# Kernel optimization log

Measured on AMD Instinct MI355X. Metric: run time of the kernel, lower is better.

## Reference

```python
import jax, jax.numpy as jnp
import numpy as np

B, T, S = 4, 2048, 2048
D, H, DFF = 1024, 16, 4096
HD = D // H
EPS = 1e-5


def layer_norm(x, gamma, beta):
    mean = x.mean(-1, keepdims=True)
    var = ((x - mean) ** 2).mean(-1, keepdims=True)
    return gamma * (x - mean) / jnp.sqrt(var + EPS) + beta


def attn(q, k, v):
    # q: [B,H,Tq,hd], k,v: [B,H,Tk,hd]
    scores = jnp.einsum('bhqd,bhkd->bhqk', q, k) / (HD ** 0.5)
    p = jax.nn.softmax(scores, axis=-1)
    return jnp.einsum('bhqk,bhkd->bhqd', p, v)


def split_heads(x, n_chunks):
    # x: [B,T,n_chunks*D] -> n_chunks tensors [B,H,T,hd] (matches torch reshape/chunk order)
    b, t, _ = x.shape
    x = x.reshape(b, t, H, n_chunks * HD).transpose(0, 2, 1, 3)
    return jnp.split(x, n_chunks, axis=-1)


def merge_heads(x):
    b, h, t, hd = x.shape
    return x.transpose(0, 2, 1, 3).reshape(b, t, h * hd)


def setup_inputs() -> dict:
    key = jax.random.key(0)
    ks = jax.random.split(key, 16)
    s = 0.02
    return {
        'x_enc': jax.random.normal(ks[0], (B, S, D), jnp.float32),
        'x_dec': jax.random.normal(ks[1], (B, T, D), jnp.float32),
        'qkv_w': jax.random.normal(ks[2], (D, 3 * D), jnp.float32) * s,
        'qkv_b': jnp.zeros((3 * D,), jnp.float32),
        'sa_o_w': jax.random.normal(ks[3], (D, D), jnp.float32) * s,
        'sa_o_b': jnp.zeros((D,), jnp.float32),
        'g1': jnp.ones((D,), jnp.float32),
        'be1': jnp.zeros((D,), jnp.float32),
        'q_w': jax.random.normal(ks[4], (D, D), jnp.float32) * s,
        'q_b': jnp.zeros((D,), jnp.float32),
        'kv_w': jax.random.normal(ks[5], (D, 2 * D), jnp.float32) * s,
        'kv_b': jnp.zeros((2 * D,), jnp.float32),
        'ca_o_w': jax.random.normal(ks[6], (D, D), jnp.float32) * s,
        'ca_o_b': jnp.zeros((D,), jnp.float32),
        'g2': jnp.ones((D,), jnp.float32),
        'be2': jnp.zeros((D,), jnp.float32),
        'ff_w1': jax.random.normal(ks[7], (D, DFF), jnp.float32) * s,
        'ff_b1': jnp.zeros((DFF,), jnp.float32),
        'ff_w2': jax.random.normal(ks[8], (DFF, D), jnp.float32) * s,
        'ff_b2': jnp.zeros((D,), jnp.float32),
        'g3': jnp.ones((D,), jnp.float32),
        'be3': jnp.zeros((D,), jnp.float32),
    }


def reference(x_enc, x_dec, qkv_w, qkv_b, sa_o_w, sa_o_b, g1, be1,
              q_w, q_b, kv_w, kv_b, ca_o_w, ca_o_b, g2, be2,
              ff_w1, ff_b1, ff_w2, ff_b2, g3, be3):
    # --- self attention on x_dec (dropout = identity at inference) ---
    qkv = x_dec @ qkv_w + qkv_b                      # [B,T,3D]
    q, k, v = split_heads(qkv, 3)
    sa = merge_heads(attn(q, k, v)) @ sa_o_w + sa_o_b
    res = layer_norm(sa + x_dec, g1, be1)
    # --- cross attention: q from decoder stream, kv from encoder ---
    kv = x_enc @ kv_w + kv_b                         # [B,S,2D]
    kc, vc = split_heads(kv, 2)
    qc, = split_heads(res @ q_w + q_b, 1)
    ca = merge_heads(attn(qc, kc, vc)) @ ca_o_w + ca_o_b
    res2 = layer_norm(ca + res, g2, be2)
    # --- feed forward ---
    ff = jax.nn.relu(res2 @ ff_w1 + ff_b1) @ ff_w2 + ff_b2
    return layer_norm(ff + res2, g3, be3)
```

## Files before the change

kernel.cpp:

```cpp
#include <hip/hip_runtime.h>

typedef unsigned short u16;
typedef unsigned int   u32;
typedef __bf16 bf16_t;
typedef bf16_t bf16x4 __attribute__((ext_vector_type(4)));
typedef bf16_t bf16x8 __attribute__((ext_vector_type(8)));
typedef float  f32x4  __attribute__((ext_vector_type(4)));

__device__ __forceinline__ u16 f2bf(float f) {
  u32 u = __builtin_bit_cast(u32, f);
  u32 r = u + 0x7fffu + ((u >> 16) & 1u);
  return (u16)(r >> 16);
}
__device__ __forceinline__ float bf2f(u16 h) {
  u32 u = ((u32)h) << 16;
  return __builtin_bit_cast(float, u);
}

__device__ __forceinline__ void gl_lds16(const u16* g, u16* l) {
  __builtin_amdgcn_global_load_lds(
      (const __attribute__((address_space(1))) u32*)g,
      (__attribute__((address_space(3))) u32*)l, 16, 0, 0);
}

__global__ __launch_bounds__(256) void k_cvt(const float* __restrict__ in,
                                             u16* __restrict__ out, long n4) {
  long i = (long)blockIdx.x * 256 + threadIdx.x;
  if (i >= n4) return;
  float4 v = reinterpret_cast<const float4*>(in)[i];
  ushort4 o;
  o.x = f2bf(v.x); o.y = f2bf(v.y); o.z = f2bf(v.z); o.w = f2bf(v.w);
  reinterpret_cast<ushort4*>(out)[i] = o;
}

__global__ __launch_bounds__(256) void k_transpose_cvt(const float* __restrict__ W,
                                                       u16* __restrict__ Wt,
                                                       int K, int N) {
  __shared__ u16 tile[32][33];
  int n0 = blockIdx.x * 32, k0 = blockIdx.y * 32;
  int tx = threadIdx.x & 31, ty = threadIdx.x >> 5;
#pragma unroll
  for (int i = 0; i < 4; ++i) {
    int k = ty + i * 8;
    tile[k][tx] = f2bf(W[(size_t)(k0 + k) * N + n0 + tx]);
  }
  __syncthreads();
#pragma unroll
  for (int i = 0; i < 4; ++i) {
    int n = ty + i * 8;
    Wt[(size_t)(n0 + n) * K + k0 + tx] = tile[tx][n];
  }
}

__global__ __launch_bounds__(256) void k_vtrans(const u16* __restrict__ in,
                                                u16* __restrict__ out,
                                                long long ibs, int ihs, int irs,
                                                int Tk) {
  __shared__ u16 t[64][72];
  const int tid = threadIdx.x;
  const int head = blockIdx.y;
  const int b = head >> 4, h = head & 15;
  const int kt = blockIdx.x * 64;
  const u16* ip = in + (size_t)b * ibs + (size_t)h * ihs;
  u16* op = out + (size_t)head * 64 * Tk;
#pragma unroll
  for (int i = 0; i < 2; ++i) {
    int c = i * 256 + tid;
    int key = c >> 3, d = (c & 7) * 8;
    *reinterpret_cast<uint4*>(&t[key][d]) =
        *reinterpret_cast<const uint4*>(ip + (size_t)(kt + key) * irs + d);
  }
  __syncthreads();
#pragma unroll
  for (int i = 0; i < 2; ++i) {
    int c = i * 256 + tid;
    int d = c >> 3, k8 = (c & 7) * 8;
    ushort4 lo, hi;
    lo.x = t[k8 + 0][d]; lo.y = t[k8 + 1][d]; lo.z = t[k8 + 2][d]; lo.w = t[k8 + 3][d];
    hi.x = t[k8 + 4][d]; hi.y = t[k8 + 5][d]; hi.z = t[k8 + 6][d]; hi.w = t[k8 + 7][d];
    uint4 o;
    o.x = ((u32)lo.y << 16) | lo.x; o.y = ((u32)lo.w << 16) | lo.z;
    o.z = ((u32)hi.y << 16) | hi.x; o.w = ((u32)hi.w << 16) | hi.z;
    *reinterpret_cast<uint4*>(op + (size_t)d * Tk + kt + k8) = o;
  }
}

template<int RELU>
__global__ __launch_bounds__(256) void k_gemm_bt(
    const u16* __restrict__ A, const u16* __restrict__ Bt,
    const float* __restrict__ bias, u16* __restrict__ C,
    int M, int N, int K)
{
  __shared__ __align__(16) u16 As[2][128 * 64];
  __shared__ __align__(16) u16 Bs[2][128 * 64];
  const int tid = threadIdx.x;
  const int lane = tid & 63, wid = tid >> 6;
  const int wr = wid >> 1, wc = wid & 1;
  const int l15 = lane & 15, g = lane >> 4;
  const int bm = blockIdx.x * 128, bn = blockIdx.y * 128;
  const int srow = lane >> 3, scol = (lane & 7) * 8;

  f32x4 acc[4][4] = {};

  auto stage = [&](int buf, int kt) {
#pragma unroll
    for (int i = 0; i < 4; ++i) {
      int ch = wid * 4 + i;
      gl_lds16(A  + (size_t)(bm + ch * 8 + srow) * K + kt + scol, &As[buf][ch * 512]);
      gl_lds16(Bt + (size_t)(bn + ch * 8 + srow) * K + kt + scol, &Bs[buf][ch * 512]);
    }
  };

  stage(0, 0);
  __syncthreads();
  int cur = 0;
  for (int kt = 0; kt < K; kt += 64) {
    if (kt + 64 < K) stage(cur ^ 1, kt + 64);
#pragma unroll
    for (int ks = 0; ks < 2; ++ks) {
      bf16x8 af[4], bfr[4];
#pragma unroll
      for (int m = 0; m < 4; ++m)
        af[m] = *reinterpret_cast<const bf16x8*>(&As[cur][(wr * 64 + m * 16 + l15) * 64 + ks * 32 + g * 8]);
#pragma unroll
      for (int n = 0; n < 4; ++n)
        bfr[n] = *reinterpret_cast<const bf16x8*>(&Bs[cur][(wc * 64 + n * 16 + l15) * 64 + ks * 32 + g * 8]);
      __builtin_amdgcn_s_setprio(1);
#pragma unroll
      for (int m = 0; m < 4; ++m)
#pragma unroll
        for (int n = 0; n < 4; ++n)
          acc[m][n] = __builtin_amdgcn_mfma_f32_16x16x32_bf16(af[m], bfr[n], acc[m][n], 0, 0, 0);
      __builtin_amdgcn_s_setprio(0);
    }
    __syncthreads();
    cur ^= 1;
  }
#pragma unroll
  for (int n = 0; n < 4; ++n) {
    int col = bn + wc * 64 + n * 16 + l15;
    float bv = bias[col];
#pragma unroll
    for (int m = 0; m < 4; ++m) {
      int row0 = bm + wr * 64 + m * 16 + g * 4;
#pragma unroll
      for (int r = 0; r < 4; ++r) {
        float v = acc[m][n][r] + bv;
        if (RELU) v = fmaxf(v, 0.f);
        C[(size_t)(row0 + r) * N + col] = f2bf(v);
      }
    }
  }
}

template<int RELU>
__global__ __launch_bounds__(512, 1) void k_gemm256(
    const u16* __restrict__ A, const u16* __restrict__ Bt,
    const float* __restrict__ bias, u16* __restrict__ C,
    int M, int N, int K)
{
  __shared__ __align__(16) u16 lds[65536];
  const int tid = threadIdx.x;
  const int lane = tid & 63, wid = tid >> 6;
  const int wr = wid >> 2, wc = wid & 3;
  const int l15 = lane & 15, g = lane >> 4;
  const int bm = blockIdx.x * 256, bn = blockIdx.y * 256;
  const int srow = tid >> 3;
  const int swcol = (((tid & 7) ^ ((tid >> 3) & 7)) * 8);
  const int swr = l15 & 7;

  f32x4 acc[8][4] = {};

  auto stageA = [&](int buf, int j, int kt) {
    gl_lds16(A + (size_t)(bm + j * 64 + srow) * K + kt + swcol,
             lds + buf * 32768 + j * 4096 + wid * 512);
  };
  auto stageB = [&](int buf, int j, int kt) {
    gl_lds16(Bt + (size_t)(bn + j * 64 + srow) * K + kt + swcol,
             lds + buf * 32768 + 16384 + j * 4096 + wid * 512);
  };

  stageB(0, 0, 0); stageB(0, 1, 0); stageB(0, 2, 0); stageB(0, 3, 0);
  stageA(0, 0, 0); stageA(0, 2, 0); stageA(0, 1, 0); stageA(0, 3, 0);
  asm volatile("s_waitcnt vmcnt(2)" ::: "memory");
  __builtin_amdgcn_s_barrier();

  int cur = 0;
  for (int kt = 0; kt < K; kt += 64) {
    const u16* Ab = lds + cur * 32768;
    const u16* Bb = lds + cur * 32768 + 16384;
    const bool pre = (kt + 64 < K);
    const int nb = cur ^ 1;
    bf16x8 af[4][2], bflo[2][2], bfhi[2][2];

#pragma unroll
    for (int m = 0; m < 4; ++m)
#pragma unroll
      for (int ks = 0; ks < 2; ++ks)
        af[m][ks] = *reinterpret_cast<const bf16x8*>(
            &Ab[(2 * wr) * 4096 + (m * 16 + l15) * 64 + (((ks * 4 + g) ^ swr) * 8)]);
#pragma unroll
    for (int n = 0; n < 2; ++n)
#pragma unroll
      for (int ks = 0; ks < 2; ++ks)
        bflo[n][ks] = *reinterpret_cast<const bf16x8*>(
            &Bb[wc * 4096 + (n * 16 + l15) * 64 + (((ks * 4 + g) ^ swr) * 8)]);
    if (pre) { stageB(nb, 0, kt + 64); stageB(nb, 1, kt + 64); }
    __builtin_amdgcn_s_setprio(1);
#pragma unroll
    for (int m = 0; m < 4; ++m)
#pragma unroll
      for (int n = 0; n < 2; ++n)
#pragma unroll
        for (int ks = 0; ks < 2; ++ks)
          acc[m][n] = __builtin_amdgcn_mfma_f32_16x16x32_bf16(af[m][ks], bflo[n][ks], acc[m][n], 0, 0, 0);
    __builtin_amdgcn_s_setprio(0);
    __builtin_amdgcn_s_barrier();

#pragma unroll
    for (int n = 0; n < 2; ++n)
#pragma unroll
      for (int ks = 0; ks < 2; ++ks)
        bfhi[n][ks] = *reinterpret_cast<const bf16x8*>(
            &Bb[wc * 4096 + ((n + 2) * 16 + l15) * 64 + (((ks * 4 + g) ^ swr) * 8)]);
    if (pre) { stageB(nb, 2, kt + 64); stageB(nb, 3, kt + 64); }
    __builtin_amdgcn_s_setprio(1);
#pragma unroll
    for (int m = 0; m < 4; ++m)
#pragma unroll
      for (int n = 0; n < 2; ++n)
#pragma unroll
        for (int ks = 0; ks < 2; ++ks)
          acc[m][n + 2] = __builtin_amdgcn_mfma_f32_16x16x32_bf16(af[m][ks], bfhi[n][ks], acc[m][n + 2], 0, 0, 0);
    __builtin_amdgcn_s_setprio(0);
    if (pre) { asm volatile("s_waitcnt vmcnt(4)" ::: "memory"); }
    else     { asm volatile("s_waitcnt vmcnt(0)" ::: "memory"); }
    __builtin_amdgcn_s_barrier();

#pragma unroll
    for (int m = 0; m < 4; ++m)
#pragma unroll
      for (int ks = 0; ks < 2; ++ks)
        af[m][ks] = *reinterpret_cast<const bf16x8*>(
            &Ab[(2 * wr + 1) * 4096 + (m * 16 + l15) * 64 + (((ks * 4 + g) ^ swr) * 8)]);
    if (pre) { stageA(nb, 0, kt + 64); stageA(nb, 2, kt + 64); }
    __builtin_amdgcn_s_setprio(1);
#pragma unroll
    for (int m = 0; m < 4; ++m)
#pragma unroll
      for (int n = 0; n < 2; ++n)
#pragma unroll
        for (int ks = 0; ks < 2; ++ks)
          acc[m + 4][n + 2] = __builtin_amdgcn_mfma_f32_16x16x32_bf16(af[m][ks], bfhi[n][ks], acc[m + 4][n + 2], 0, 0, 0);
    __builtin_amdgcn_s_setprio(0);
    __builtin_amdgcn_s_barrier();

    if (pre) { stageA(nb, 1, kt + 64); stageA(nb, 3, kt + 64); }
    __builtin_amdgcn_s_setprio(1);
#pragma unroll
    for (int m = 0; m < 4; ++m)
#pragma unroll
      for (int n = 0; n < 2; ++n)
#pragma unroll
        for (int ks = 0; ks < 2; ++ks)
          acc[m + 4][n] = __builtin_amdgcn_mfma_f32_16x16x32_bf16(af[m][ks], bflo[n][ks], acc[m + 4][n], 0, 0, 0);
    __builtin_amdgcn_s_setprio(0);
    asm volatile("s_waitcnt vmcnt(2)" ::: "memory");
    __builtin_amdgcn_s_barrier();
    cur ^= 1;
  }

#pragma unroll
  for (int n = 0; n < 4; ++n) {
    int col = bn + wc * 64 + n * 16 + l15;
    float bv = bias[col];
#pragma unroll
    for (int m = 0; m < 8; ++m) {
      int row0 = bm + wr * 128 + m * 16 + g * 4;
#pragma unroll
      for (int r = 0; r < 4; ++r) {
        float v = acc[m][n][r] + bv;
        if (RELU) v = fmaxf(v, 0.f);
        C[(size_t)(row0 + r) * N + col] = f2bf(v);
      }
    }
  }
}

__global__ __launch_bounds__(256) void k_flash2(
    const u16* __restrict__ Qg, const u16* __restrict__ Kg, const u16* __restrict__ VTg,
    u16* __restrict__ Og,
    long long qbs, int qhs, int qrs,
    long long kbs, int khs, int krs,
    long long obs, int ohs, int ors,
    int Tk)
{
  __shared__ __align__(16) u16 Ks[64][72];
  __shared__ __align__(16) u16 Vs[64][72];
  __shared__ __align__(16) u16 Ps0[4][16][72];
  __shared__ __align__(16) u16 Ps1[4][16][72];
  const int tid = threadIdx.x;
  const int lane = tid & 63, wid = tid >> 6;
  const int l15 = lane & 15, g = lane >> 4;
  const int head = blockIdx.x;
  const int b = head >> 4, h = head & 15;
  const int srow = tid >> 3, scol = (tid & 7) * 8;

  const u16* Q  = Qg + (size_t)b * qbs + (size_t)h * qhs;
  const u16* Kp = Kg + (size_t)b * kbs + (size_t)h * khs;
  const u16* Vp = VTg + (size_t)head * 64 * Tk;
  u16* Op = Og + (size_t)b * obs + (size_t)h * ohs;

  const int q0 = blockIdx.y * 128 + wid * 32;
  const float SCL = 0.125f * 1.44269504f;

  bf16x8 qf0[2], qf1[2];
#pragma unroll
  for (int ks = 0; ks < 2; ++ks) {
    bf16x8 r0 = *reinterpret_cast<const bf16x8*>(Q + (size_t)(q0 + l15) * qrs + ks * 32 + g * 8);
    bf16x8 r1 = *reinterpret_cast<const bf16x8*>(Q + (size_t)(q0 + 16 + l15) * qrs + ks * 32 + g * 8);
#pragma unroll
    for (int j = 0; j < 8; ++j) {
      qf0[ks][j] = (bf16_t)((float)r0[j] * SCL);
      qf1[ks][j] = (bf16_t)((float)r1[j] * SCL);
    }
  }
  bf16x8 ones;
#pragma unroll
  for (int j = 0; j < 8; ++j) ones[j] = (bf16_t)1.0f;

  f32x4 oacc0[4] = {}, oacc1[4] = {};
  f32x4 lacc0 = {}, lacc1 = {};

  uint4 ka0, ka1, va0, va1, kb0, kb1, vb0, vb1;

  auto load_set = [&](int kt, uint4& k0, uint4& k1, uint4& v0, uint4& v1) {
    k0 = *reinterpret_cast<const uint4*>(Kp + (size_t)(kt + srow) * krs + scol);
    k1 = *reinterpret_cast<const uint4*>(Kp + (size_t)(kt + srow + 32) * krs + scol);
    v0 = *reinterpret_cast<const uint4*>(Vp + (size_t)srow * Tk + kt + scol);
    v1 = *reinterpret_cast<const uint4*>(Vp + (size_t)(srow + 32) * Tk + kt + scol);
  };

  auto tile = [&](const uint4& k0, const uint4& k1, const uint4& v0, const uint4& v1,
                  int ktn, uint4& nk0, uint4& nk1, uint4& nv0, uint4& nv1) {
    __syncthreads();
    *reinterpret_cast<uint4*>(&Ks[srow][scol])      = k0;
    *reinterpret_cast<uint4*>(&Ks[srow + 32][scol]) = k1;
    *reinterpret_cast<uint4*>(&Vs[srow][scol])      = v0;
    *reinterpret_cast<uint4*>(&Vs[srow + 32][scol]) = v1;
    load_set(ktn, nk0, nk1, nv0, nv1);
    __syncthreads();

    f32x4 sc0[4] = {}, sc1[4] = {};
    __builtin_amdgcn_s_setprio(1);
#pragma unroll
    for (int ks = 0; ks < 2; ++ks)
#pragma unroll
      for (int kb = 0; kb < 4; ++kb) {
        bf16x8 kf = *reinterpret_cast<const bf16x8*>(&Ks[kb * 16 + l15][ks * 32 + g * 8]);
        sc0[kb] = __builtin_amdgcn_mfma_f32_16x16x32_bf16(kf, qf0[ks], sc0[kb], 0, 0, 0);
        sc1[kb] = __builtin_amdgcn_mfma_f32_16x16x32_bf16(kf, qf1[ks], sc1[kb], 0, 0, 0);
      }
    __builtin_amdgcn_s_setprio(0);

#pragma unroll
    for (int kb = 0; kb < 4; ++kb) {
      bf16x4 pk0, pk1;
#pragma unroll
      for (int r = 0; r < 4; ++r) {
        pk0[r] = (bf16_t)__builtin_amdgcn_exp2f(sc0[kb][r]);
        pk1[r] = (bf16_t)__builtin_amdgcn_exp2f(sc1[kb][r]);
      }
      *reinterpret_cast<bf16x4*>(&Ps0[wid][l15][kb * 16 + g * 4]) = pk0;
      *reinterpret_cast<bf16x4*>(&Ps1[wid][l15][kb * 16 + g * 4]) = pk1;
    }
    asm volatile("s_waitcnt lgkmcnt(0)" ::: "memory");
#pragma unroll
    for (int kc = 0; kc < 2; ++kc) {
      bf16x8 pf0 = *reinterpret_cast<const bf16x8*>(&Ps0[wid][l15][kc * 32 + g * 8]);
      bf16x8 pf1 = *reinterpret_cast<const bf16x8*>(&Ps1[wid][l15][kc * 32 + g * 8]);
      __builtin_amdgcn_s_setprio(1);
#pragma unroll
      for (int nb = 0; nb < 4; ++nb) {
        bf16x8 vf = *reinterpret_cast<const bf16x8*>(&Vs[nb * 16 + l15][kc * 32 + g * 8]);
        oacc0[nb] = __builtin_amdgcn_mfma_f32_16x16x32_bf16(pf0, vf, oacc0[nb], 0, 0, 0);
        oacc1[nb] = __builtin_amdgcn_mfma_f32_16x16x32_bf16(pf1, vf, oacc1[nb], 0, 0, 0);
      }
      lacc0 = __builtin_amdgcn_mfma_f32_16x16x32_bf16(pf0, ones, lacc0, 0, 0, 0);
      lacc1 = __builtin_amdgcn_mfma_f32_16x16x32_bf16(pf1, ones, lacc1, 0, 0, 0);
      __builtin_amdgcn_s_setprio(0);
    }
  };

  load_set(0, ka0, ka1, va0, va1);
  for (int kt = 0; kt < Tk; kt += 128) {
    tile(ka0, ka1, va0, va1, kt + 64, kb0, kb1, vb0, vb1);
    int ktn = (kt + 128 < Tk) ? kt + 128 : 0;
    tile(kb0, kb1, vb0, vb1, ktn, ka0, ka1, va0, va1);
  }

#pragma unroll
  for (int r = 0; r < 4; ++r) {
    float inv0 = 1.f / lacc0[r];
    float inv1 = 1.f / lacc1[r];
#pragma unroll
    for (int nb = 0; nb < 4; ++nb) {
      Op[(size_t)(q0 + g * 4 + r) * ors + nb * 16 + l15]      = f2bf(oacc0[nb][r] * inv0);
      Op[(size_t)(q0 + 16 + g * 4 + r) * ors + nb * 16 + l15] = f2bf(oacc1[nb][r] * inv1);
    }
  }
}

__device__ __forceinline__ void load4v(const float* p, float* v) {
  float4 t = *reinterpret_cast<const float4*>(p);
  v[0] = t.x; v[1] = t.y; v[2] = t.z; v[3] = t.w;
}
__device__ __forceinline__ void load4v(const u16* p, float* v) {
  ushort4 t = *reinterpret_cast<const ushort4*>(p);
  v[0] = bf2f(t.x); v[1] = bf2f(t.y); v[2] = bf2f(t.z); v[3] = bf2f(t.w);
}
__device__ __forceinline__ void store4v(float* p, const float* v) {
  float4 t; t.x = v[0]; t.y = v[1]; t.z = v[2]; t.w = v[3];
  *reinterpret_cast<float4*>(p) = t;
}
__device__ __forceinline__ void store4v(u16* p, const float* v) {
  ushort4 t; t.x = f2bf(v[0]); t.y = f2bf(v[1]); t.z = f2bf(v[2]); t.w = f2bf(v[3]);
  *reinterpret_cast<ushort4*>(p) = t;
}

template<typename TRES, typename TOUT>
__global__ __launch_bounds__(256) void k_add_ln(
    const u16* __restrict__ X, const TRES* __restrict__ R,
    const float* __restrict__ gamma, const float* __restrict__ beta,
    TOUT* __restrict__ Out)
{
  const int row = blockIdx.x;
  const int tid = threadIdx.x;
  const size_t base = (size_t)row * 1024 + tid * 4;
  float x[4], rr[4];
  load4v(X + base, x);
  load4v(R + base, rr);
  float v[4];
#pragma unroll
  for (int j = 0; j < 4; ++j) v[j] = x[j] + rr[j];
  float s = v[0] + v[1] + v[2] + v[3];
  float q = v[0]*v[0] + v[1]*v[1] + v[2]*v[2] + v[3]*v[3];
#pragma unroll
  for (int off = 32; off > 0; off >>= 1) {
    s += __shfl_down(s, off);
    q += __shfl_down(q, off);
  }
  __shared__ float sh[8];
  const int lane = tid & 63, wid = tid >> 6;
  if (lane == 0) { sh[wid] = s; sh[4 + wid] = q; }
  __syncthreads();
  s = sh[0] + sh[1] + sh[2] + sh[3];
  q = sh[4] + sh[5] + sh[6] + sh[7];
  float mean = s * (1.f / 1024.f);
  float var = q * (1.f / 1024.f) - mean * mean;
  float inv = 1.f / sqrtf(var + 1e-5f);
  float gv[4], bv[4], o[4];
  load4v(gamma + tid * 4, gv);
  load4v(beta + tid * 4, bv);
#pragma unroll
  for (int j = 0; j < 4; ++j) o[j] = gv[j] * (v[j] - mean) * inv + bv[j];
  store4v(Out + base, o);
}

extern "C" void kernel_launch(void* const* d_in, const int* in_sizes, int n_in,
                              void* d_out, int out_size, void* d_ws, size_t ws_size,
                              hipStream_t stream)
{
  (void)in_sizes; (void)n_in; (void)out_size; (void)ws_size;
  const float* x_enc  = (const float*)d_in[0];
  const float* x_dec  = (const float*)d_in[1];
  const float* qkv_w  = (const float*)d_in[2];
  const float* qkv_b  = (const float*)d_in[3];
  const float* sa_o_w = (const float*)d_in[4];
  const float* sa_o_b = (const float*)d_in[5];
  const float* g1     = (const float*)d_in[6];
  const float* be1    = (const float*)d_in[7];
  const float* q_w    = (const float*)d_in[8];
  const float* q_b    = (const float*)d_in[9];
  const float* kv_w   = (const float*)d_in[10];
  const float* kv_b   = (const float*)d_in[11];
  const float* ca_o_w = (const float*)d_in[12];
  const float* ca_o_b = (const float*)d_in[13];
  const float* g2     = (const float*)d_in[14];
  const float* be2    = (const float*)d_in[15];
  const float* ff_w1  = (const float*)d_in[16];
  const float* ff_b1  = (const float*)d_in[17];
  const float* ff_w2  = (const float*)d_in[18];
  const float* ff_b2  = (const float*)d_in[19];
  const float* g3     = (const float*)d_in[20];
  const float* be3    = (const float*)d_in[21];
  float* out = (float*)d_out;

  u16* Wb = (u16*)d_ws;
  const size_t O_WQKV = 0;
  const size_t O_WSAO = O_WQKV + (size_t)3072 * 1024;
  const size_t O_WQ   = O_WSAO + (size_t)1024 * 1024;
  const size_t O_WKV  = O_WQ   + (size_t)1024 * 1024;
  const size_t O_WCAO = O_WKV  + (size_t)2048 * 1024;
  const size_t O_WFF1 = O_WCAO + (size_t)1024 * 1024;
  const size_t O_WFF2 = O_WFF1 + (size_t)4096 * 1024;
  const size_t O_XD   = O_WFF2 + (size_t)1024 * 4096;
  const size_t O_XE   = O_XD + 8388608;
  const size_t O_QKV  = O_XE + 8388608;
  const size_t O_QC   = O_QKV + 16777216;
  const size_t O_ATT  = O_QKV + 25165824;
  const size_t O_RES  = O_ATT + 8388608;
  const size_t O_RES2 = O_RES + 8388608;
  const size_t O_FF1  = O_RES2 + 8388608;
  const size_t O_VT   = O_FF1;
  const size_t O_VT2  = O_FF1 + 8388608;
  const size_t O_GO   = O_FF1 + 33554432;

  k_cvt<<<8192, 256, 0, stream>>>(x_dec, Wb + O_XD, 2097152);
  k_cvt<<<8192, 256, 0, stream>>>(x_enc, Wb + O_XE, 2097152);
  k_transpose_cvt<<<dim3(96, 32),  256, 0, stream>>>(qkv_w,  Wb + O_WQKV, 1024, 3072);
  k_transpose_cvt<<<dim3(32, 32),  256, 0, stream>>>(sa_o_w, Wb + O_WSAO, 1024, 1024);
  k_transpose_cvt<<<dim3(32, 32),  256, 0, stream>>>(q_w,    Wb + O_WQ,   1024, 1024);
  k_transpose_cvt<<<dim3(64, 32),  256, 0, stream>>>(kv_w,   Wb + O_WKV,  1024, 2048);
  k_transpose_cvt<<<dim3(32, 32),  256, 0, stream>>>(ca_o_w, Wb + O_WCAO, 1024, 1024);
  k_transpose_cvt<<<dim3(128, 32), 256, 0, stream>>>(ff_w1,  Wb + O_WFF1, 1024, 4096);
  k_transpose_cvt<<<dim3(32, 128), 256, 0, stream>>>(ff_w2,  Wb + O_WFF2, 4096, 1024);

  k_gemm256<0><<<dim3(32, 12), 512, 0, stream>>>(Wb + O_XD, Wb + O_WQKV, qkv_b,
                                                 Wb + O_QKV, 8192, 3072, 1024);
  k_vtrans<<<dim3(32, 64), 256, 0, stream>>>(Wb + O_QKV + 128, Wb + O_VT,
                                             (long long)2048 * 3072, 192, 3072, 2048);
  k_flash2<<<dim3(64, 16), 256, 0, stream>>>(Wb + O_QKV, Wb + O_QKV + 64, Wb + O_VT,
                                             Wb + O_ATT,
                                             (long long)2048 * 3072, 192, 3072,
                                             (long long)2048 * 3072, 192, 3072,
                                             (long long)2048 * 1024, 64, 1024, 2048);
  k_gemm_bt<0><<<dim3(64, 8), 256, 0, stream>>>(Wb + O_ATT, Wb + O_WSAO, sa_o_b,
                                                Wb + O_GO, 8192, 1024, 1024);
  k_add_ln<float, u16><<<8192, 256, 0, stream>>>(Wb + O_GO, x_dec, g1, be1, Wb + O_RES);

  k_gemm256<0><<<dim3(32, 8), 512, 0, stream>>>(Wb + O_XE, Wb + O_WKV, kv_b,
                                                Wb + O_QKV, 8192, 2048, 1024);
  k_vtrans<<<dim3(32, 64), 256, 0, stream>>>(Wb + O_QKV + 64, Wb + O_VT2,
                                             (long long)2048 * 2048, 128, 2048, 2048);
  k_gemm_bt<0><<<dim3(64, 8), 256, 0, stream>>>(Wb + O_RES, Wb + O_WQ, q_b,
                                                Wb + O_QC, 8192, 1024, 1024);
  k_flash2<<<dim3(64, 16), 256, 0, stream>>>(Wb + O_QC, Wb + O_QKV, Wb + O_VT2,
                                             Wb + O_ATT,
                                             (long long)2048 * 1024, 64, 1024,
                                             (long long)2048 * 2048, 128, 2048,
                                             (long long)2048 * 1024, 64, 1024, 2048);
  k_gemm_bt<0><<<dim3(64, 8), 256, 0, stream>>>(Wb + O_ATT, Wb + O_WCAO, ca_o_b,
                                                Wb + O_GO, 8192, 1024, 1024);
  k_add_ln<u16, u16><<<8192, 256, 0, stream>>>(Wb + O_GO, Wb + O_RES, g2, be2, Wb + O_RES2);

  k_gemm256<1><<<dim3(32, 16), 512, 0, stream>>>(Wb + O_RES2, Wb + O_WFF1, ff_b1,
                                                 Wb + O_FF1, 8192, 4096, 1024);
  k_gemm_bt<0><<<dim3(64, 8), 256, 0, stream>>>(Wb + O_FF1, Wb + O_WFF2, ff_b2,
                                                Wb + O_GO, 8192, 1024, 4096);
  k_add_ln<u16, float><<<8192, 256, 0, stream>>>(Wb + O_GO, Wb + O_RES2, g3, be3, out);
}
```

Measured before the change: 657.6 us.

## Split-K the FF2 GEMM and fuse partial-sum reduction into final LayerNorm

The second feed-forward GEMM (K=4096) now runs as a split-K kernel with two K chunks, doubling the grid to 1024 blocks and writing fp32 partials to the workspace. The final add+LayerNorm kernel sums the two partials, the bias and the residual before normalising. This targets low occupancy and a long serial K loop in the 512-block GEMM, at the cost of extra fp32 partial traffic (two 32MB buffers written and read) instead of a bf16 output.

Result: no change. 658.6 us (+0.2%).

```diff
diff --git a/kernel.cpp b/kernel.cpp
--- a/kernel.cpp
+++ b/kernel.cpp
@@ -149,6 +149,69 @@
         if (RELU) v = fmaxf(v, 0.f);
         C[(size_t)(row0 + r) * N + col] = f2bf(v);
       }
+    }
+  }
+}
+
+__global__ __launch_bounds__(256) void k_gemm_sk(
+    const u16* __restrict__ A, const u16* __restrict__ Bt,
+    float* __restrict__ P,
+    int M, int N, int Kfull, int Kchunk)
+{
+  __shared__ __align__(16) u16 As[2][128 * 32];
+  __shared__ __align__(16) u16 Bs[2][128 * 32];
+  const int tid = threadIdx.x;
+  const int lane = tid & 63, wid = tid >> 6;
+  const int wr = wid >> 1, wc = wid & 1;
+  const int l15 = lane & 15, g = lane >> 4;
+  const int bm = blockIdx.x * 128, bn = blockIdx.y * 128;
+  const int z = blockIdx.z;
+  const int k0 = z * Kchunk;
+  float* Pz = P + (size_t)z * M * N;
+  const int srow = tid >> 2, scol = (tid & 3) * 8;
+
+  f32x4 acc[4][4] = {};
+
+  auto stage = [&](int buf, int kt) {
+#pragma unroll
+    for (int i = 0; i < 2; ++i) {
+      int row = i * 64 + srow;
+      gl_lds16(A  + (size_t)(bm + row) * Kfull + k0 + kt + scol, &As[buf][row * 32 + scol]);
+      gl_lds16(Bt + (size_t)(bn + row) * Kfull + k0 + kt + scol, &Bs[buf][row * 32 + scol]);
+    }
+  };
+
+  stage(0, 0);
+  __syncthreads();
+  int cur = 0;
+  for (int kt = 0; kt < Kchunk; kt += 32) {
+    if (kt + 32 < Kchunk) stage(cur ^ 1, kt + 32);
+    bf16x8 af[4], bfr[4];
+#pragma unroll
+    for (int m = 0; m < 4; ++m)
+      af[m] = *reinterpret_cast<const bf16x8*>(&As[cur][(wr * 64 + m * 16 + l15) * 32 + g * 8]);
+#pragma unroll
+    for (int n = 0; n < 4; ++n)
+      bfr[n] = *reinterpret_cast<const bf16x8*>(&Bs[cur][(wc * 64 + n * 16 + l15) * 32 + g * 8]);
+    __builtin_amdgcn_s_setprio(1);
+#pragma unroll
+    for (int m = 0; m < 4; ++m)
+#pragma unroll
+      for (int n = 0; n < 4; ++n)
+        acc[m][n] = __builtin_amdgcn_mfma_f32_16x16x32_bf16(af[m], bfr[n], acc[m][n], 0, 0, 0);
+    __builtin_amdgcn_s_setprio(0);
+    __syncthreads();
+    cur ^= 1;
+  }
+#pragma unroll
+  for (int n = 0; n < 4; ++n) {
+    int col = bn + wc * 64 + n * 16 + l15;
+#pragma unroll
+    for (int m = 0; m < 4; ++m) {
+      int row0 = bm + wr * 64 + m * 16 + g * 4;
+#pragma unroll
+      for (int r = 0; r < 4; ++r)
+        Pz[(size_t)(row0 + r) * N + col] = acc[m][n][r];
     }
   }
 }
@@ -428,6 +491,31 @@
   *reinterpret_cast<ushort4*>(p) = t;
 }
 
+__device__ __forceinline__ void ln_core(float* v, int tid, const float* gamma,
+                                        const float* beta, float* o) {
+  float s = v[0] + v[1] + v[2] + v[3];
+  float q = v[0]*v[0] + v[1]*v[1] + v[2]*v[2] + v[3]*v[3];
+#pragma unroll
+  for (int off = 32; off > 0; off >>= 1) {
+    s += __shfl_down(s, off);
+    q += __shfl_down(q, off);
+  }
+  __shared__ float sh[8];
+  const int lane = tid & 63, wid = tid >> 6;
+  if (lane == 0) { sh[wid] = s; sh[4 + wid] = q; }
+  __syncthreads();
+  s = sh[0] + sh[1] + sh[2] + sh[3];
+  q = sh[4] + sh[5] + sh[6] + sh[7];
+  float mean = s * (1.f / 1024.f);
+  float var = q * (1.f / 1024.f) - mean * mean;
+  float inv = 1.f / sqrtf(var + 1e-5f);
+  float gv[4], bv[4];
+  load4v(gamma + tid * 4, gv);
+  load4v(beta + tid * 4, bv);
+#pragma unroll
+  for (int j = 0; j < 4; ++j) o[j] = gv[j] * (v[j] - mean) * inv + bv[j];
+}
+
 template<typename TRES, typename TOUT>
 __global__ __launch_bounds__(256) void k_add_ln(
     const u16* __restrict__ X, const TRES* __restrict__ R,
@@ -437,33 +525,32 @@
   const int row = blockIdx.x;
   const int tid = threadIdx.x;
   const size_t base = (size_t)row * 1024 + tid * 4;
-  float x[4], rr[4];
+  float x[4], rr[4], v[4], o[4];
   load4v(X + base, x);
   load4v(R + base, rr);
-  float v[4];
 #pragma unroll
   for (int j = 0; j < 4; ++j) v[j] = x[j] + rr[j];
-  float s = v[0] + v[1] + v[2] + v[3];
-  float q = v[0]*v[0] + v[1]*v[1] + v[2]*v[2] + v[3]*v[3];
-#pragma unroll
-  for (int off = 32; off > 0; off >>= 1) {
-    s += __shfl_down(s, off);
-    q += __shfl_down(q, off);
-  }
-  __shared__ float sh[8];
-  const int lane = tid & 63, wid = tid >> 6;
-  if (lane == 0) { sh[wid] = s; sh[4 + wid] = q; }
-  __syncthreads();
-  s = sh[0] + sh[1] + sh[2] + sh[3];
-  q = sh[4] + sh[5] + sh[6] + sh[7];
-  float mean = s * (1.f / 1024.f);
-  float var = q * (1.f / 1024.f) - mean * mean;
-  float inv = 1.f / sqrtf(var + 1e-5f);
-  float gv[4], bv[4], o[4];
-  load4v(gamma + tid * 4, gv);
-  load4v(beta + tid * 4, bv);
-#pragma unroll
-  for (int j = 0; j < 4; ++j) o[j] = gv[j] * (v[j] - mean) * inv + bv[j];
+  ln_core(v, tid, gamma, beta, o);
+  store4v(Out + base, o);
+}
+
+__global__ __launch_bounds__(256) void k_add_ln_ff(
+    const float* __restrict__ P0, const float* __restrict__ P1,
+    const float* __restrict__ bias, const u16* __restrict__ R,
+    const float* __restrict__ gamma, const float* __restrict__ beta,
+    float* __restrict__ Out)
+{
+  const int row = blockIdx.x;
+  const int tid = threadIdx.x;
+  const size_t base = (size_t)row * 1024 + tid * 4;
+  float p0[4], p1[4], bb[4], rr[4], v[4], o[4];
+  load4v(P0 + base, p0);
+  load4v(P1 + base, p1);
+  load4v(bias + tid * 4, bb);
+  load4v(R + base, rr);
+#pragma unroll
+  for (int j = 0; j < 4; ++j) v[j] = p0[j] + p1[j] + bb[j] + rr[j];
+  ln_core(v, tid, gamma, beta, o);
   store4v(Out + base, o);
 }
 
@@ -515,6 +602,7 @@
   const size_t O_VT   = O_FF1;
   const size_t O_VT2  = O_FF1 + 8388608;
   const size_t O_GO   = O_FF1 + 33554432;
+  float* Pf = (float*)(Wb + O_QKV);
 
   k_cvt<<<8192, 256, 0, stream>>>(x_dec, Wb + O_XD, 2097152);
   k_cvt<<<8192, 256, 0, stream>>>(x_enc, Wb + O_XE, 2097152);
@@ -556,7 +644,8 @@
 
   k_gemm256<1><<<dim3(32, 16), 512, 0, stream>>>(Wb + O_RES2, Wb + O_WFF1, ff_b1,
                                                  Wb + O_FF1, 8192, 4096, 1024);
-  k_gemm_bt<0><<<dim3(64, 8), 256, 0, stream>>>(Wb + O_FF1, Wb + O_WFF2, ff_b2,
-                                                Wb + O_GO, 8192, 1024, 4096);
-  k_add_ln<u16, float><<<8192, 256, 0, stream>>>(Wb + O_GO, Wb + O_RES2, g3, be3, out);
-}
+  k_gemm_sk<<<dim3(64, 8, 2), 256, 0, stream>>>(Wb + O_FF1, Wb + O_WFF2, Pf,
+                                                8192, 1024, 4096, 2048);
+  k_add_ln_ff<<<8192, 256, 0, stream>>>(Pf, Pf + 8388608, ff_b2, Wb + O_RES2,
+                                        g3, be3, out);
+}
```
